# Kernel optimization log

Hardware: AMD Instinct MI355X
Metric: run time of the kernel (lower is better)

The kernel has to match this reference:

```python
import jax, jax.numpy as jnp
import numpy as np

DIM_M = 512
NEG_INF = -1e30


def setup_inputs() -> dict:
    key = jax.random.key(0)
    k1, k2, k3, k4, k5, k6, k7 = jax.random.split(key, 7)
    B, Lc, Lq, d = 16, 1024, 512, DIM_M
    C = jax.random.normal(k1, (B, Lc, d), dtype=jnp.float32)
    Q = jax.random.normal(k2, (B, Lq, d), dtype=jnp.float32)
    cmask = jax.random.randint(k3, (B, Lc), 0, 2).astype(jnp.float32)
    qmask = jax.random.randint(k4, (B, Lq), 0, 2).astype(jnp.float32)
    lim = np.sqrt(1.0 / d)
    w = jax.random.uniform(k5, (3 * d,), minval=-lim, maxval=lim, dtype=jnp.float32)
    # out_linear: Linear(4d -> d), torch default init
    bound = np.sqrt(1.0 / (4 * d))
    out_w = jax.random.uniform(k6, (d, 4 * d), minval=-bound, maxval=bound, dtype=jnp.float32)
    out_b = jax.random.uniform(k7, (d,), minval=-bound, maxval=bound, dtype=jnp.float32)
    return {"C": C, "Q": Q, "cmask": cmask, "qmask": qmask, "w": w, "out_w": out_w, "out_b": out_b}


def _mask_logits(t, m):
    return t * m + (1.0 - m) * NEG_INF


def reference(C, Q, cmask, qmask, w, out_w, out_b):
    d = C.shape[-1]
    w1, w2, w3 = w[:d], w[d:2 * d], w[2 * d:]
    # Decomposed trilinear similarity (same math as cat([Ct,Qt,Ct*Qt]) @ w):
    # S[b,i,j] = C[b,i]@w1 + Q[b,j]@w2 + (C[b,i]*w3) @ Q[b,j]
    S = (C @ w1)[:, :, None] + (Q @ w2)[:, None, :] \
        + jnp.einsum('bid,bjd->bij', C * w3, Q)  # [B, Lc, Lq]
    qm = qmask[:, None, :]  # [B, 1, Lq]
    cm = cmask[:, :, None]  # [B, Lc, 1]
    S1 = jax.nn.softmax(_mask_logits(S, qm), axis=2)  # over Lq
    S2 = jax.nn.softmax(_mask_logits(S, cm), axis=1)  # over Lc
    A = jnp.einsum('bij,bjd->bid', S1, Q)  # [B, Lc, d]
    # bmm(bmm(S1, S2^T), C) == S1 @ (S2^T @ C) by associativity (cheaper)
    S2TC = jnp.einsum('bij,bid->bjd', S2, C)  # [B, Lq, d]
    Bm = jnp.einsum('bij,bjd->bid', S1, S2TC)  # [B, Lc, d]
    out = jnp.concatenate([C, A, C * A, C * Bm], axis=2)  # [B, Lc, 4d]
    # dropout inactive (inference); out_linear
    return out @ out_w.T + out_b
```

## Files before the change

kernel.cpp:

```cpp
#include <hip/hip_runtime.h>
#include <hip/hip_bf16.h>


#define NB 16
#define LC 1024
#define LQ 512
#define DM 512
#define D4 2048
#define NEGINF (-1e30f)
#define LDA64 72
#define LDA32 40

typedef __bf16 v8bf __attribute__((ext_vector_type(8)));
typedef __bf16 v4bf __attribute__((ext_vector_type(4)));
typedef float  v4f  __attribute__((ext_vector_type(4)));

#define MFMA16 __builtin_amdgcn_mfma_f32_16x16x32_bf16

#define TILE_SETUP8 \
  const int t = threadIdx.x, lane = t & 63, wave = t >> 6; \
  const int wm = wave >> 2, wn = wave & 3, quad = lane >> 4, col = lane & 15;

#define ZERO_ACC8 \
  v4f acc[4][2]; \
  _Pragma("unroll") for (int x = 0; x < 4; ++x) \
  _Pragma("unroll") for (int y = 0; y < 2; ++y) \
  _Pragma("unroll") for (int r = 0; r < 4; ++r) acc[x][y][r] = 0.f;

#define FRAG_MMA8S(AL, BL, LDA, KO) do { \
  v8bf af_[4], bf_[2]; \
  _Pragma("unroll") for (int x = 0; x < 4; ++x) \
    af_[x] = *(const v8bf*)&AL[(wm * 64 + x * 16 + col) * LDA + KO + quad * 8]; \
  _Pragma("unroll") for (int y = 0; y < 2; ++y) \
    bf_[y] = *(const v8bf*)&BL[(wn * 32 + y * 16 + col) * LDA + KO + quad * 8]; \
  _Pragma("unroll") for (int x = 0; x < 4; ++x) \
  _Pragma("unroll") for (int y = 0; y < 2; ++y) \
    acc[x][y] = MFMA16(af_[x], bf_[y], acc[x][y], 0, 0, 0); \
} while (0)

#define TILE_SETUP4 \
  const int t = threadIdx.x, lane = t & 63, wave = t >> 6; \
  const int wm = wave >> 1, wn = wave & 1, quad = lane >> 4, col = lane & 15;

#define ZERO_ACC4 \
  v4f acc[4][4]; \
  _Pragma("unroll") for (int x = 0; x < 4; ++x) \
  _Pragma("unroll") for (int y = 0; y < 4; ++y) \
  _Pragma("unroll") for (int r = 0; r < 4; ++r) acc[x][y][r] = 0.f;

#define FRAG_MMA4(AL, BL, LDA, KO) do { \
  v8bf af_[4], bf_[4]; \
  _Pragma("unroll") for (int x = 0; x < 4; ++x) \
    af_[x] = *(const v8bf*)&AL[(wm * 64 + x * 16 + col) * LDA + KO + quad * 8]; \
  _Pragma("unroll") for (int y = 0; y < 4; ++y) \
    bf_[y] = *(const v8bf*)&BL[(wn * 64 + y * 16 + col) * LDA + KO + quad * 8]; \
  _Pragma("unroll") for (int x = 0; x < 4; ++x) \
  _Pragma("unroll") for (int y = 0; y < 4; ++y) \
    acc[x][y] = MFMA16(af_[x], bf_[y], acc[x][y], 0, 0, 0); \
} while (0)

__device__ __forceinline__ void xcd_remap(int& bx, int& by, int& bz) {
  const int gx = gridDim.x, gy = gridDim.y, gz = gridDim.z;
  int flat = bx + gx * (by + gy * bz);
  int per = (gx * gy * gz) >> 3;
  int nw = (flat & 7) * per + (flat >> 3);
  bx = nw % gx;
  int r = nw / gx;
  by = r % gy;
  bz = r / gy;
}

__device__ __forceinline__ v8bf cvt8f(float4 a, float4 b) {
  v8bf h;
  h[0] = (__bf16)a.x; h[1] = (__bf16)a.y; h[2] = (__bf16)a.z; h[3] = (__bf16)a.w;
  h[4] = (__bf16)b.x; h[5] = (__bf16)b.y; h[6] = (__bf16)b.z; h[7] = (__bf16)b.w;
  return h;
}

__global__ void k_transpose(const float* __restrict__ in, __bf16* __restrict__ outT,
                            int R, int Cd) {
  __shared__ __bf16 tile[64][66];
  const int b = blockIdx.z;
  const int r0 = blockIdx.y * 64, c0 = blockIdx.x * 64;
  const float* inb = in + (size_t)b * R * Cd;
  __bf16* outb = outT + (size_t)b * Cd * R;
  const int rr = threadIdx.x >> 4, c4 = (threadIdx.x & 15) * 4;
#pragma unroll
  for (int p = 0; p < 4; ++p) {
    const int r = rr + p * 16;
    float4 f = *(const float4*)(inb + (size_t)(r0 + r) * Cd + c0 + c4);
    tile[r][c4 + 0] = (__bf16)f.x; tile[r][c4 + 1] = (__bf16)f.y;
    tile[r][c4 + 2] = (__bf16)f.z; tile[r][c4 + 3] = (__bf16)f.w;
  }
  __syncthreads();
  const int c = threadIdx.x & 63, rb = (threadIdx.x >> 6) * 4;
#pragma unroll
  for (int p = 0; p < 4; ++p) {
    const int r4 = rb + p * 16;
    v4bf h;
#pragma unroll
    for (int e = 0; e < 4; ++e) h[e] = tile[r4 + e][c];
    *(v4bf*)(outb + (size_t)(c0 + c) * R + r0 + r4) = h;
  }
}

__global__ void k_owcvt(const float* __restrict__ OW, __bf16* __restrict__ OWb) {
  size_t i = ((size_t)blockIdx.x * 256 + threadIdx.x) * 4;
  float4 f = *(const float4*)(OW + i);
  v4bf h; h[0] = (__bf16)f.x; h[1] = (__bf16)f.y; h[2] = (__bf16)f.z; h[3] = (__bf16)f.w;
  *(v4bf*)(OWb + i) = h;
}

__global__ __launch_bounds__(512) void k_mfma_S(
    const float* __restrict__ C, const float* __restrict__ Q, const float* __restrict__ w,
    float* __restrict__ S) {
  __shared__ __bf16 Al[128 * LDA64], Bl[128 * LDA64];
  __shared__ float cwL[128], qwL[128];
  int bx = blockIdx.x, by = blockIdx.y, bz = blockIdx.z;
  xcd_remap(bx, by, bz);
  const int b = bz, i0 = by * 128, j0 = bx * 128;
  TILE_SETUP8
  const int sr = t >> 2, skc = (t & 3) * 16;
  const float* Cb = C + (size_t)b * LC * DM;
  const float* Qb = Q + (size_t)b * LQ * DM;
  const float* w1 = w, *w2 = w + DM, *w3 = w + 2 * DM;
  float4 pc[4], pq[4];
  auto load = [&](int k0) {
    const float* ca = Cb + (size_t)(i0 + sr) * DM + k0 + skc;
    const float* qa = Qb + (size_t)(j0 + sr) * DM + k0 + skc;
#pragma unroll
    for (int u = 0; u < 4; ++u) {
      pc[u] = *(const float4*)(ca + 4 * u);
      pq[u] = *(const float4*)(qa + 4 * u);
    }
  };
  load(0);
  ZERO_ACC8
  float cdot = 0.f, qdot = 0.f;
  for (int k0 = 0; k0 < DM; k0 += 64) {
#pragma unroll
    for (int u = 0; u < 2; ++u) {
      float4 c0 = pc[2 * u], c1 = pc[2 * u + 1];
      float4 q0 = pq[2 * u], q1 = pq[2 * u + 1];
      const float* w3a = w3 + k0 + skc + 8 * u;
      float4 w30 = *(const float4*)w3a, w31 = *(const float4*)(w3a + 4);
      const float* w1a = w1 + k0 + skc + 8 * u;
      float4 w10 = *(const float4*)w1a, w11 = *(const float4*)(w1a + 4);
      const float* w2a = w2 + k0 + skc + 8 * u;
      float4 w20 = *(const float4*)w2a, w21 = *(const float4*)(w2a + 4);
      v8bf ah;
      ah[0] = (__bf16)(c0.x * w30.x); ah[1] = (__bf16)(c0.y * w30.y);
      ah[2] = (__bf16)(c0.z * w30.z); ah[3] = (__bf16)(c0.w * w30.w);
      ah[4] = (__bf16)(c1.x * w31.x); ah[5] = (__bf16)(c1.y * w31.y);
      ah[6] = (__bf16)(c1.z * w31.z); ah[7] = (__bf16)(c1.w * w31.w);
      *(v8bf*)&Al[sr * LDA64 + skc + 8 * u] = ah;
      *(v8bf*)&Bl[sr * LDA64 + skc + 8 * u] = cvt8f(q0, q1);
      cdot += c0.x * w10.x + c0.y * w10.y + c0.z * w10.z + c0.w * w10.w
            + c1.x * w11.x + c1.y * w11.y + c1.z * w11.z + c1.w * w11.w;
      qdot += q0.x * w20.x + q0.y * w20.y + q0.z * w20.z + q0.w * w20.w
            + q1.x * w21.x + q1.y * w21.y + q1.z * w21.z + q1.w * w21.w;
    }
    __syncthreads();
    int kn = k0 + 64; if (kn >= DM) kn = 0;
    load(kn);
    FRAG_MMA8S(Al, Bl, LDA64, 0);
    FRAG_MMA8S(Al, Bl, LDA64, 32);
    __syncthreads();
  }
  cdot += __shfl_xor(cdot, 1); cdot += __shfl_xor(cdot, 2);
  qdot += __shfl_xor(qdot, 1); qdot += __shfl_xor(qdot, 2);
  if ((t & 3) == 0) { cwL[sr] = cdot; qwL[sr] = qdot; }
  __syncthreads();
  float* Sb = S + (size_t)b * LC * LQ;
#pragma unroll
  for (int x = 0; x < 4; ++x) {
    const int ml = wm * 64 + x * 16 + quad * 4;
    float cv[4];
#pragma unroll
    for (int r = 0; r < 4; ++r) cv[r] = cwL[ml + r];
#pragma unroll
    for (int y = 0; y < 2; ++y) {
      const int jl = wn * 32 + y * 16 + col;
      const float qv = qwL[jl];
#pragma unroll
      for (int r = 0; r < 4; ++r)
        Sb[(size_t)(i0 + ml + r) * LQ + j0 + jl] = acc[x][y][r] + cv[r] + qv;
    }
  }
}

__global__ __launch_bounds__(1024) void k_softstat(
    const float* __restrict__ S, const float* __restrict__ qmask,
    const float* __restrict__ cmask, __bf16* __restrict__ S1,
    float2* __restrict__ pstat) {
  __shared__ float2 cst[16][LQ];
  const int b = blockIdx.y, ic = blockIdx.x;
  const int tid = threadIdx.x, wv = tid >> 6, lane = tid & 63;
  const int jb = lane * 8;
  const float* qm  = qmask + b * LQ;
  const float* cm  = cmask + b * LC + ic * 64;
  const float* Sb  = S  + ((size_t)b * LC + ic * 64) * LQ;
  __bf16*      S1b = S1 + ((size_t)b * LC + ic * 64) * LQ;
  float qv[8];
  {
    float4 q0 = *(const float4*)(qm + jb), q1 = *(const float4*)(qm + jb + 4);
    qv[0] = q0.x; qv[1] = q0.y; qv[2] = q0.z; qv[3] = q0.w;
    qv[4] = q1.x; qv[5] = q1.y; qv[6] = q1.z; qv[7] = q1.w;
  }
  float colm[8], cols[8];
#pragma unroll
  for (int e = 0; e < 8; ++e) { colm[e] = -3e38f; cols[e] = 0.f; }
  for (int it = 0; it < 4; ++it) {
    const int r = wv * 4 + it;
    const float cmv = cm[r];
    const float* Srow = Sb + (size_t)r * LQ + jb;
    float4 s0 = *(const float4*)Srow, s1 = *(const float4*)(Srow + 4);
    float sv[8] = {s0.x, s0.y, s0.z, s0.w, s1.x, s1.y, s1.z, s1.w};
    float l1[8];
    float m = -3e38f;
#pragma unroll
    for (int e = 0; e < 8; ++e) {
      l1[e] = qv[e] * sv[e] + (1.f - qv[e]) * NEGINF;
      m = fmaxf(m, l1[e]);
    }
#pragma unroll
    for (int off = 32; off; off >>= 1) m = fmaxf(m, __shfl_xor(m, off, 64));
    float ex[8], s = 0.f;
#pragma unroll
    for (int e = 0; e < 8; ++e) { ex[e] = __expf(l1[e] - m); s += ex[e]; }
#pragma unroll
    for (int off = 32; off; off >>= 1) s += __shfl_xor(s, off, 64);
    const float inv = 1.f / s;
    v8bf h;
#pragma unroll
    for (int e = 0; e < 8; ++e) h[e] = (__bf16)(ex[e] * inv);
    *(v8bf*)(S1b + (size_t)r * LQ + jb) = h;
#pragma unroll
    for (int e = 0; e < 8; ++e) {
      float l2 = cmv * sv[e] + (1.f - cmv) * NEGINF;
      if (l2 > colm[e]) { cols[e] *= __expf(colm[e] - l2); colm[e] = l2; }
      cols[e] += __expf(l2 - colm[e]);
    }
  }
#pragma unroll
  for (int e = 0; e < 8; ++e) cst[wv][jb + e] = make_float2(colm[e], cols[e]);
  __syncthreads();
  if (tid < LQ) {
    float M = -3e38f, Sd = 0.f;
#pragma unroll
    for (int k = 0; k < 16; ++k) {
      float2 p = cst[k][tid];
      float nM = fmaxf(M, p.x);
      Sd = Sd * __expf(M - nM) + p.y * __expf(p.x - nM);
      M = nM;
    }
    pstat[((size_t)(b * 16 + ic) * LQ) + tid] = make_float2(M, Sd);
  }
}

__global__ void k_colwrite(const float* __restrict__ S, const float* __restrict__ cmask,
                           const float2* __restrict__ pstat, __bf16* __restrict__ S2T) {
  __shared__ float Mf[64], If[64];
  __shared__ __bf16 tile[64][66];
  const int b = blockIdx.z, ic = blockIdx.y, j0 = blockIdx.x * 64;
  if (threadIdx.x < 64) {
    float M = -3e38f, Sd = 0.f;
#pragma unroll
    for (int k = 0; k < 16; ++k) {
      float2 p = pstat[((size_t)(b * 16 + k) * LQ) + j0 + threadIdx.x];
      float nM = fmaxf(M, p.x);
      Sd = Sd * __expf(M - nM) + p.y * __expf(p.x - nM);
      M = nM;
    }
    Mf[threadIdx.x] = M; If[threadIdx.x] = 1.f / Sd;
  }
  __syncthreads();
  const float* Sb = S + ((size_t)b * LC + ic * 64) * LQ;
  const float* cm = cmask + b * LC + ic * 64;
  const int rr = threadIdx.x >> 4, c4 = (threadIdx.x & 15) * 4;
#pragma unroll
  for (int p = 0; p < 4; ++p) {
    const int r = rr + p * 16;
    const float mk = cm[r];
    float4 sv = *(const float4*)(Sb + (size_t)r * LQ + j0 + c4);
    float s[4] = {sv.x, sv.y, sv.z, sv.w};
#pragma unroll
    for (int e = 0; e < 4; ++e) {
      float logit = mk * s[e] + (1.f - mk) * NEGINF;
      tile[r][c4 + e] = (__bf16)(__expf(logit - Mf[c4 + e]) * If[c4 + e]);
    }
  }
  __syncthreads();
  __bf16* S2Tb = S2T + ((size_t)b * LQ + j0) * LC + ic * 64;
  const int c = threadIdx.x & 63, rb = (threadIdx.x >> 6) * 4;
#pragma unroll
  for (int p = 0; p < 4; ++p) {
    const int r4 = rb + p * 16;
    v4bf h;
#pragma unroll
    for (int e = 0; e < 4; ++e) h[e] = tile[r4 + e][c];
    *(v4bf*)(S2Tb + (size_t)c * LC + r4) = h;
  }
}

__global__ __launch_bounds__(256) void k_mfma_A(
    const __bf16* __restrict__ S1, const __bf16* __restrict__ QT, __bf16* __restrict__ Aw) {
  __shared__ __bf16 Al[128 * LDA64], Bl[128 * LDA64];
  int bx = blockIdx.x, by = blockIdx.y, bz = blockIdx.z;
  xcd_remap(bx, by, bz);
  const int b = bz, i0 = by * 128, n0 = bx * 128;
  TILE_SETUP4
  const int sr = t >> 1, kh = (t & 1) * 32;
  const __bf16* Ar = S1 + (size_t)b * LC * LQ + (size_t)(i0 + sr) * LQ + kh;
  const __bf16* Br = QT + (size_t)b * DM * LQ + (size_t)(n0 + sr) * LQ + kh;
  v8bf pa[4], pb[4];
  auto load = [&](int k0) {
#pragma unroll
    for (int u = 0; u < 4; ++u) {
      pa[u] = *(const v8bf*)(Ar + k0 + 8 * u);
      pb[u] = *(const v8bf*)(Br + k0 + 8 * u);
    }
  };
  load(0);
  ZERO_ACC4
  for (int k0 = 0; k0 < LQ; k0 += 64) {
#pragma unroll
    for (int u = 0; u < 4; ++u) {
      *(v8bf*)&Al[sr * LDA64 + kh + 8 * u] = pa[u];
      *(v8bf*)&Bl[sr * LDA64 + kh + 8 * u] = pb[u];
    }
    __syncthreads();
    int kn = k0 + 64; if (kn >= LQ) kn = 0;
    load(kn);
    FRAG_MMA4(Al, Bl, LDA64, 0);
    FRAG_MMA4(Al, Bl, LDA64, 32);
    __syncthreads();
  }
  __bf16* Ab = Aw + (size_t)b * LC * DM;
#pragma unroll
  for (int x = 0; x < 4; ++x) {
    const int mB = i0 + wm * 64 + x * 16 + quad * 4;
#pragma unroll
    for (int y = 0; y < 4; ++y) {
      const int n = n0 + wn * 64 + y * 16 + col;
#pragma unroll
      for (int r = 0; r < 4; ++r)
        Ab[(size_t)(mB + r) * DM + n] = (__bf16)acc[x][y][r];
    }
  }
}

__global__ __launch_bounds__(512) void k_mfma_T(
    const __bf16* __restrict__ S2T, const __bf16* __restrict__ CT, __bf16* __restrict__ S2TCT) {
  __shared__ __bf16 Al[128 * LDA64], Bl[128 * LDA64];
  int bx = blockIdx.x, by = blockIdx.y, bz = blockIdx.z;
  xcd_remap(bx, by, bz);
  const int b = bz, j0 = by * 128, n0 = bx * 128;
  TILE_SETUP8
  const int sr = t >> 2, skc = (t & 3) * 16;
  const __bf16* Ar = S2T + (size_t)b * LQ * LC + (size_t)(j0 + sr) * LC + skc;
  const __bf16* Br = CT  + (size_t)b * DM * LC + (size_t)(n0 + sr) * LC + skc;
  v8bf pa0, pa1, pb0, pb1;
  auto load = [&](int k0) {
    pa0 = *(const v8bf*)(Ar + k0); pa1 = *(const v8bf*)(Ar + k0 + 8);
    pb0 = *(const v8bf*)(Br + k0); pb1 = *(const v8bf*)(Br + k0 + 8);
  };
  load(0);
  ZERO_ACC8
  for (int k0 = 0; k0 < LC; k0 += 64) {
    *(v8bf*)&Al[sr * LDA64 + skc] = pa0; *(v8bf*)&Al[sr * LDA64 + skc + 8] = pa1;
    *(v8bf*)&Bl[sr * LDA64 + skc] = pb0; *(v8bf*)&Bl[sr * LDA64 + skc + 8] = pb1;
    __syncthreads();
    int kn = k0 + 64; if (kn >= LC) kn = 0;
    load(kn);
    FRAG_MMA8S(Al, Bl, LDA64, 0);
    FRAG_MMA8S(Al, Bl, LDA64, 32);
    __syncthreads();
  }
#pragma unroll
  for (int x = 0; x < 4; ++x) {
    const int jB = j0 + wm * 64 + x * 16 + quad * 4;
#pragma unroll
    for (int y = 0; y < 2; ++y) {
      const int n = n0 + wn * 32 + y * 16 + col;
      v4bf h;
#pragma unroll
      for (int r = 0; r < 4; ++r) h[r] = (__bf16)acc[x][y][r];
      *(v4bf*)&S2TCT[((size_t)b * DM + n) * LQ + jB] = h;
    }
  }
}

__global__ __launch_bounds__(256) void k_mfma_Bm(
    const __bf16* __restrict__ S1, const __bf16* __restrict__ S2TCT, __bf16* __restrict__ Bmw) {
  __shared__ __bf16 Al[128 * LDA64], Bl[128 * LDA64];
  int bx = blockIdx.x, by = blockIdx.y, bz = blockIdx.z;
  xcd_remap(bx, by, bz);
  const int b = bz, i0 = by * 128, n0 = bx * 128;
  TILE_SETUP4
  const int sr = t >> 1, kh = (t & 1) * 32;
  const __bf16* Ar = S1    + (size_t)b * LC * LQ + (size_t)(i0 + sr) * LQ + kh;
  const __bf16* Br = S2TCT + (size_t)b * DM * LQ + (size_t)(n0 + sr) * LQ + kh;
  v8bf pa[4], pb[4];
  auto load = [&](int k0) {
#pragma unroll
    for (int u = 0; u < 4; ++u) {
      pa[u] = *(const v8bf*)(Ar + k0 + 8 * u);
      pb[u] = *(const v8bf*)(Br + k0 + 8 * u);
    }
  };
  load(0);
  ZERO_ACC4
  for (int k0 = 0; k0 < LQ; k0 += 64) {
#pragma unroll
    for (int u = 0; u < 4; ++u) {
      *(v8bf*)&Al[sr * LDA64 + kh + 8 * u] = pa[u];
      *(v8bf*)&Bl[sr * LDA64 + kh + 8 * u] = pb[u];
    }
    __syncthreads();
    int kn = k0 + 64; if (kn >= LQ) kn = 0;
    load(kn);
    FRAG_MMA4(Al, Bl, LDA64, 0);
    FRAG_MMA4(Al, Bl, LDA64, 32);
    __syncthreads();
  }
  __bf16* Bb = Bmw + (size_t)b * LC * DM;
#pragma unroll
  for (int x = 0; x < 4; ++x) {
    const int mB = i0 + wm * 64 + x * 16 + quad * 4;
#pragma unroll
    for (int y = 0; y < 4; ++y) {
      const int n = n0 + wn * 64 + y * 16 + col;
#pragma unroll
      for (int r = 0; r < 4; ++r)
        Bb[(size_t)(mB + r) * DM + n] = (__bf16)acc[x][y][r];
    }
  }
}

__global__ __launch_bounds__(256) void k_mfma_out(
    const float* __restrict__ C, const __bf16* __restrict__ Aw, const __bf16* __restrict__ Bmw,
    const __bf16* __restrict__ OWb, const float* __restrict__ ob, float* __restrict__ out) {
  __shared__ __bf16 Asg[4][128 * LDA32], Bsg[4][128 * LDA32];
  int bx = blockIdx.x, by = blockIdx.y, bz = blockIdx.z;
  xcd_remap(bx, by, bz);
  const int b = bz, i0 = by * 128, n0 = bx * 128;
  TILE_SETUP4
  const int sr = t >> 1, kh = (t & 1) * 16;
  const float*  Cr = C   + (size_t)b * LC * DM + (size_t)(i0 + sr) * DM + kh;
  const __bf16* Ar = Aw  + (size_t)b * LC * DM + (size_t)(i0 + sr) * DM + kh;
  const __bf16* Br = Bmw + (size_t)b * LC * DM + (size_t)(i0 + sr) * DM + kh;
  const __bf16* Wr = OWb + (size_t)(n0 + sr) * D4 + kh;
  float4 pc[4]; v8bf pA[2], pB[2], pw[4][2];
  auto load = [&](int kl) {
#pragma unroll
    for (int u = 0; u < 4; ++u) pc[u] = *(const float4*)(Cr + kl + 4 * u);
#pragma unroll
    for (int u = 0; u < 2; ++u) {
      pA[u] = *(const v8bf*)(Ar + kl + 8 * u);
      pB[u] = *(const v8bf*)(Br + kl + 8 * u);
    }
#pragma unroll
    for (int s = 0; s < 4; ++s)
#pragma unroll
      for (int u = 0; u < 2; ++u) pw[s][u] = *(const v8bf*)(Wr + s * DM + kl + 8 * u);
  };
  load(0);
  ZERO_ACC4
  for (int kl = 0; kl < DM; kl += 32) {
#pragma unroll
    for (int u = 0; u < 2; ++u) {
      float4 f0 = pc[2 * u], f1 = pc[2 * u + 1];
      float cf[8] = {f0.x, f0.y, f0.z, f0.w, f1.x, f1.y, f1.z, f1.w};
      v8bf hC, hCA, hCB;
#pragma unroll
      for (int e = 0; e < 8; ++e) {
        hC[e]  = (__bf16)cf[e];
        hCA[e] = (__bf16)(cf[e] * (float)pA[u][e]);
        hCB[e] = (__bf16)(cf[e] * (float)pB[u][e]);
      }
      const int off = sr * LDA32 + kh + 8 * u;
      *(v8bf*)&Asg[0][off] = hC;
      *(v8bf*)&Asg[1][off] = pA[u];
      *(v8bf*)&Asg[2][off] = hCA;
      *(v8bf*)&Asg[3][off] = hCB;
#pragma unroll
      for (int s = 0; s < 4; ++s) *(v8bf*)&Bsg[s][off] = pw[s][u];
    }
    __syncthreads();
    int kn = kl + 32; if (kn >= DM) kn = 0;
    load(kn);
#pragma unroll
    for (int s = 0; s < 4; ++s) FRAG_MMA4(Asg[s], Bsg[s], LDA32, 0);
    __syncthreads();
  }
  float* outb = out + (size_t)b * LC * DM;
#pragma unroll
  for (int x = 0; x < 4; ++x) {
    const int mB = i0 + wm * 64 + x * 16 + quad * 4;
#pragma unroll
    for (int y = 0; y < 4; ++y) {
      const int n = n0 + wn * 64 + y * 16 + col;
      const float bv = ob[n];
#pragma unroll
      for (int r = 0; r < 4; ++r)
        outb[(size_t)(mB + r) * DM + n] = acc[x][y][r] + bv;
    }
  }
}

extern "C" void kernel_launch(void* const* d_in, const int* in_sizes, int n_in,
                              void* d_out, int out_size, void* d_ws, size_t ws_size,
                              hipStream_t stream) {
  const float* C     = (const float*)d_in[0];
  const float* Q     = (const float*)d_in[1];
  const float* cmask = (const float*)d_in[2];
  const float* qmask = (const float*)d_in[3];
  const float* w     = (const float*)d_in[4];
  const float* out_w = (const float*)d_in[5];
  const float* out_b = (const float*)d_in[6];
  float* out = (float*)d_out;

  char* base = (char*)d_ws;
  char*   R     = base + 131072;
  float*  S     = (float*)R;
  __bf16* Aw    = (__bf16*)R;
  __bf16* CT    = (__bf16*)(R + (16u << 20));
  __bf16* Bmw   = (__bf16*)(R + (16u << 20));
  __bf16* S1    = (__bf16*)(base + 131072 + (32u << 20));
  __bf16* S2T   = (__bf16*)(base + 131072 + (48u << 20));
  __bf16* OWbf  = S2T;
  char*   Z     = base + 131072 + (64u << 20);
  float2* pstat = (float2*)Z;
  __bf16* QT    = (__bf16*)Z;
  __bf16* S2TCT = (__bf16*)Z;
  (void)in_sizes; (void)n_in; (void)out_size; (void)ws_size;

  k_mfma_S<<<dim3(LQ / 128, LC / 128, NB), 512, 0, stream>>>(C, Q, w, S);
  k_softstat<<<dim3(LC / 64, NB), 1024, 0, stream>>>(S, qmask, cmask, S1, pstat);
  k_colwrite<<<dim3(LQ / 64, LC / 64, NB), 256, 0, stream>>>(S, cmask, pstat, S2T);
  k_transpose<<<dim3(DM / 64, LQ / 64, NB), 256, 0, stream>>>(Q, QT, LQ, DM);
  k_transpose<<<dim3(DM / 64, LC / 64, NB), 256, 0, stream>>>(C, CT, LC, DM);
  k_mfma_A<<<dim3(DM / 128, LC / 128, NB), 256, 0, stream>>>(S1, QT, Aw);
  k_mfma_T<<<dim3(DM / 128, LQ / 128, NB), 512, 0, stream>>>(S2T, CT, S2TCT);
  k_owcvt<<<DM * D4 / 1024, 256, 0, stream>>>(out_w, OWbf);
  k_mfma_Bm<<<dim3(DM / 128, LC / 128, NB), 256, 0, stream>>>(S1, S2TCT, Bmw);
  k_mfma_out<<<dim3(DM / 128, LC / 128, NB), 256, 0, stream>>>(C, Aw, Bmw, OWbf, out_b, out);
}
```

Baseline: 315.5 us.

## Use 8-wave tiles for GEMMs and pre-swizzle out_w into MFMA fragment layout

Switches k_mfma_A, k_mfma_Bm and k_mfma_out from 4-wave 64x64 warp tiles to 8-wave 64x32 tiles with 512-thread blocks, halving per-thread accumulators and staging loads. out_w is now pre-converted into MFMA B-fragment order, so k_mfma_out reads weight fragments directly from global memory/cache instead of staging them through LDS. This cuts LDS footprint and traffic. Transpose writes are widened to 16-byte stores. The trade-off is more weight fragment loads from global memory per wave, and smaller per-wave tiles with lower reuse.

```diff
diff --git a/kernel.cpp b/kernel.cpp
--- a/kernel.cpp
+++ b/kernel.cpp
@@ -38,27 +38,6 @@
     acc[x][y] = MFMA16(af_[x], bf_[y], acc[x][y], 0, 0, 0); \
 } while (0)
 
-#define TILE_SETUP4 \
-  const int t = threadIdx.x, lane = t & 63, wave = t >> 6; \
-  const int wm = wave >> 1, wn = wave & 1, quad = lane >> 4, col = lane & 15;
-
-#define ZERO_ACC4 \
-  v4f acc[4][4]; \
-  _Pragma("unroll") for (int x = 0; x < 4; ++x) \
-  _Pragma("unroll") for (int y = 0; y < 4; ++y) \
-  _Pragma("unroll") for (int r = 0; r < 4; ++r) acc[x][y][r] = 0.f;
-
-#define FRAG_MMA4(AL, BL, LDA, KO) do { \
-  v8bf af_[4], bf_[4]; \
-  _Pragma("unroll") for (int x = 0; x < 4; ++x) \
-    af_[x] = *(const v8bf*)&AL[(wm * 64 + x * 16 + col) * LDA + KO + quad * 8]; \
-  _Pragma("unroll") for (int y = 0; y < 4; ++y) \
-    bf_[y] = *(const v8bf*)&BL[(wn * 64 + y * 16 + col) * LDA + KO + quad * 8]; \
-  _Pragma("unroll") for (int x = 0; x < 4; ++x) \
-  _Pragma("unroll") for (int y = 0; y < 4; ++y) \
-    acc[x][y] = MFMA16(af_[x], bf_[y], acc[x][y], 0, 0, 0); \
-} while (0)
-
 __device__ __forceinline__ void xcd_remap(int& bx, int& by, int& bz) {
   const int gx = gridDim.x, gy = gridDim.y, gz = gridDim.z;
   int flat = bx + gx * (by + gy * bz);
@@ -93,22 +72,23 @@
     tile[r][c4 + 2] = (__bf16)f.z; tile[r][c4 + 3] = (__bf16)f.w;
   }
   __syncthreads();
-  const int c = threadIdx.x & 63, rb = (threadIdx.x >> 6) * 4;
-#pragma unroll
-  for (int p = 0; p < 4; ++p) {
-    const int r4 = rb + p * 16;
-    v4bf h;
-#pragma unroll
-    for (int e = 0; e < 4; ++e) h[e] = tile[r4 + e][c];
-    *(v4bf*)(outb + (size_t)(c0 + c) * R + r0 + r4) = h;
-  }
-}
-
-__global__ void k_owcvt(const float* __restrict__ OW, __bf16* __restrict__ OWb) {
-  size_t i = ((size_t)blockIdx.x * 256 + threadIdx.x) * 4;
-  float4 f = *(const float4*)(OW + i);
-  v4bf h; h[0] = (__bf16)f.x; h[1] = (__bf16)f.y; h[2] = (__bf16)f.z; h[3] = (__bf16)f.w;
-  *(v4bf*)(OWb + i) = h;
+  const int cc = threadIdx.x >> 2, r16 = (threadIdx.x & 3) * 16;
+  v8bf h0, h1;
+#pragma unroll
+  for (int e = 0; e < 8; ++e) { h0[e] = tile[r16 + e][cc]; h1[e] = tile[r16 + 8 + e][cc]; }
+  *(v8bf*)(outb + (size_t)(c0 + cc) * R + r0 + r16) = h0;
+  *(v8bf*)(outb + (size_t)(c0 + cc) * R + r0 + r16 + 8) = h1;
+}
+
+__global__ void k_owfrag(const float* __restrict__ OW, __bf16* __restrict__ Wf) {
+  const int gid = blockIdx.x * 256 + threadIdx.x;
+  const int lane = gid & 63, f = gid >> 6;
+  const int nt = f >> 6, kc = f & 63;
+  const int n = nt * 16 + (lane & 15);
+  const int k = kc * 32 + (lane >> 4) * 8;
+  const float* src = OW + (size_t)n * D4 + k;
+  float4 a = *(const float4*)src, b = *(const float4*)(src + 4);
+  *(v8bf*)(Wf + (size_t)f * 512 + lane * 8) = cvt8f(a, b);
 }
 
 __global__ __launch_bounds__(512) void k_mfma_S(
@@ -292,48 +272,39 @@
   }
   __syncthreads();
   __bf16* S2Tb = S2T + ((size_t)b * LQ + j0) * LC + ic * 64;
-  const int c = threadIdx.x & 63, rb = (threadIdx.x >> 6) * 4;
-#pragma unroll
-  for (int p = 0; p < 4; ++p) {
-    const int r4 = rb + p * 16;
-    v4bf h;
-#pragma unroll
-    for (int e = 0; e < 4; ++e) h[e] = tile[r4 + e][c];
-    *(v4bf*)(S2Tb + (size_t)c * LC + r4) = h;
-  }
-}
-
-__global__ __launch_bounds__(256) void k_mfma_A(
+  const int jj = threadIdx.x >> 2, i16 = (threadIdx.x & 3) * 16;
+  v8bf h0, h1;
+#pragma unroll
+  for (int e = 0; e < 8; ++e) { h0[e] = tile[i16 + e][jj]; h1[e] = tile[i16 + 8 + e][jj]; }
+  *(v8bf*)(S2Tb + (size_t)jj * LC + i16) = h0;
+  *(v8bf*)(S2Tb + (size_t)jj * LC + i16 + 8) = h1;
+}
+
+__global__ __launch_bounds__(512) void k_mfma_A(
     const __bf16* __restrict__ S1, const __bf16* __restrict__ QT, __bf16* __restrict__ Aw) {
   __shared__ __bf16 Al[128 * LDA64], Bl[128 * LDA64];
   int bx = blockIdx.x, by = blockIdx.y, bz = blockIdx.z;
   xcd_remap(bx, by, bz);
   const int b = bz, i0 = by * 128, n0 = bx * 128;
-  TILE_SETUP4
-  const int sr = t >> 1, kh = (t & 1) * 32;
-  const __bf16* Ar = S1 + (size_t)b * LC * LQ + (size_t)(i0 + sr) * LQ + kh;
-  const __bf16* Br = QT + (size_t)b * DM * LQ + (size_t)(n0 + sr) * LQ + kh;
-  v8bf pa[4], pb[4];
+  TILE_SETUP8
+  const int sr = t >> 2, skc = (t & 3) * 16;
+  const __bf16* Ar = S1 + (size_t)b * LC * LQ + (size_t)(i0 + sr) * LQ + skc;
+  const __bf16* Br = QT + (size_t)b * DM * LQ + (size_t)(n0 + sr) * LQ + skc;
+  v8bf pa0, pa1, pb0, pb1;
   auto load = [&](int k0) {
-#pragma unroll
-    for (int u = 0; u < 4; ++u) {
-      pa[u] = *(const v8bf*)(Ar + k0 + 8 * u);
-      pb[u] = *(const v8bf*)(Br + k0 + 8 * u);
-    }
+    pa0 = *(const v8bf*)(Ar + k0); pa1 = *(const v8bf*)(Ar + k0 + 8);
+    pb0 = *(const v8bf*)(Br + k0); pb1 = *(const v8bf*)(Br + k0 + 8);
   };
   load(0);
-  ZERO_ACC4
+  ZERO_ACC8
   for (int k0 = 0; k0 < LQ; k0 += 64) {
-#pragma unroll
-    for (int u = 0; u < 4; ++u) {
-      *(v8bf*)&Al[sr * LDA64 + kh + 8 * u] = pa[u];
-      *(v8bf*)&Bl[sr * LDA64 + kh + 8 * u] = pb[u];
-    }
+    *(v8bf*)&Al[sr * LDA64 + skc] = pa0; *(v8bf*)&Al[sr * LDA64 + skc + 8] = pa1;
+    *(v8bf*)&Bl[sr * LDA64 + skc] = pb0; *(v8bf*)&Bl[sr * LDA64 + skc + 8] = pb1;
     __syncthreads();
     int kn = k0 + 64; if (kn >= LQ) kn = 0;
     load(kn);
-    FRAG_MMA4(Al, Bl, LDA64, 0);
-    FRAG_MMA4(Al, Bl, LDA64, 32);
+    FRAG_MMA8S(Al, Bl, LDA64, 0);
+    FRAG_MMA8S(Al, Bl, LDA64, 32);
     __syncthreads();
   }
   __bf16* Ab = Aw + (size_t)b * LC * DM;
@@ -341,8 +312,8 @@
   for (int x = 0; x < 4; ++x) {
     const int mB = i0 + wm * 64 + x * 16 + quad * 4;
 #pragma unroll
-    for (int y = 0; y < 4; ++y) {
-      const int n = n0 + wn * 64 + y * 16 + col;
+    for (int y = 0; y < 2; ++y) {
+      const int n = n0 + wn * 32 + y * 16 + col;
 #pragma unroll
       for (int r = 0; r < 4; ++r)
         Ab[(size_t)(mB + r) * DM + n] = (__bf16)acc[x][y][r];
@@ -391,37 +362,31 @@
   }
 }
 
-__global__ __launch_bounds__(256) void k_mfma_Bm(
+__global__ __launch_bounds__(512) void k_mfma_Bm(
     const __bf16* __restrict__ S1, const __bf16* __restrict__ S2TCT, __bf16* __restrict__ Bmw) {
   __shared__ __bf16 Al[128 * LDA64], Bl[128 * LDA64];
   int bx = blockIdx.x, by = blockIdx.y, bz = blockIdx.z;
   xcd_remap(bx, by, bz);
   const int b = bz, i0 = by * 128, n0 = bx * 128;
-  TILE_SETUP4
-  const int sr = t >> 1, kh = (t & 1) * 32;
-  const __bf16* Ar = S1    + (size_t)b * LC * LQ + (size_t)(i0 + sr) * LQ + kh;
-  const __bf16* Br = S2TCT + (size_t)b * DM * LQ + (size_t)(n0 + sr) * LQ + kh;
-  v8bf pa[4], pb[4];
+  TILE_SETUP8
+  const int sr = t >> 2, skc = (t & 3) * 16;
+  const __bf16* Ar = S1    + (size_t)b * LC * LQ + (size_t)(i0 + sr) * LQ + skc;
+  const __bf16* Br = S2TCT + (size_t)b * DM * LQ + (size_t)(n0 + sr) * LQ + skc;
+  v8bf pa0, pa1, pb0, pb1;
   auto load = [&](int k0) {
-#pragma unroll
-    for (int u = 0; u < 4; ++u) {
-      pa[u] = *(const v8bf*)(Ar + k0 + 8 * u);
-      pb[u] = *(const v8bf*)(Br + k0 + 8 * u);
-    }
+    pa0 = *(const v8bf*)(Ar + k0); pa1 = *(const v8bf*)(Ar + k0 + 8);
+    pb0 = *(const v8bf*)(Br + k0); pb1 = *(const v8bf*)(Br + k0 + 8);
   };
   load(0);
-  ZERO_ACC4
+  ZERO_ACC8
   for (int k0 = 0; k0 < LQ; k0 += 64) {
-#pragma unroll
-    for (int u = 0; u < 4; ++u) {
-      *(v8bf*)&Al[sr * LDA64 + kh + 8 * u] = pa[u];
-      *(v8bf*)&Bl[sr * LDA64 + kh + 8 * u] = pb[u];
-    }
+    *(v8bf*)&Al[sr * LDA64 + skc] = pa0; *(v8bf*)&Al[sr * LDA64 + skc + 8] = pa1;
+    *(v8bf*)&Bl[sr * LDA64 + skc] = pb0; *(v8bf*)&Bl[sr * LDA64 + skc + 8] = pb1;
     __syncthreads();
     int kn = k0 + 64; if (kn >= LQ) kn = 0;
     load(kn);
-    FRAG_MMA4(Al, Bl, LDA64, 0);
-    FRAG_MMA4(Al, Bl, LDA64, 32);
+    FRAG_MMA8S(Al, Bl, LDA64, 0);
+    FRAG_MMA8S(Al, Bl, LDA64, 32);
     __syncthreads();
   }
   __bf16* Bb = Bmw + (size_t)b * LC * DM;
@@ -429,8 +394,8 @@
   for (int x = 0; x < 4; ++x) {
     const int mB = i0 + wm * 64 + x * 16 + quad * 4;
 #pragma unroll
-    for (int y = 0; y < 4; ++y) {
-      const int n = n0 + wn * 64 + y * 16 + col;
+    for (int y = 0; y < 2; ++y) {
+      const int n = n0 + wn * 32 + y * 16 + col;
 #pragma unroll
       for (int r = 0; r < 4; ++r)
         Bb[(size_t)(mB + r) * DM + n] = (__bf16)acc[x][y][r];
@@ -438,60 +403,64 @@
   }
 }
 
-__global__ __launch_bounds__(256) void k_mfma_out(
+__global__ __launch_bounds__(512) void k_mfma_out(
     const float* __restrict__ C, const __bf16* __restrict__ Aw, const __bf16* __restrict__ Bmw,
-    const __bf16* __restrict__ OWb, const float* __restrict__ ob, float* __restrict__ out) {
-  __shared__ __bf16 Asg[4][128 * LDA32], Bsg[4][128 * LDA32];
+    const __bf16* __restrict__ Wf, const float* __restrict__ ob, float* __restrict__ out) {
+  __shared__ __bf16 Asg[4][128 * LDA32];
   int bx = blockIdx.x, by = blockIdx.y, bz = blockIdx.z;
   xcd_remap(bx, by, bz);
   const int b = bz, i0 = by * 128, n0 = bx * 128;
-  TILE_SETUP4
-  const int sr = t >> 1, kh = (t & 1) * 16;
-  const float*  Cr = C   + (size_t)b * LC * DM + (size_t)(i0 + sr) * DM + kh;
-  const __bf16* Ar = Aw  + (size_t)b * LC * DM + (size_t)(i0 + sr) * DM + kh;
-  const __bf16* Br = Bmw + (size_t)b * LC * DM + (size_t)(i0 + sr) * DM + kh;
-  const __bf16* Wr = OWb + (size_t)(n0 + sr) * D4 + kh;
-  float4 pc[4]; v8bf pA[2], pB[2], pw[4][2];
+  TILE_SETUP8
+  const int sr = t >> 2, skc = (t & 3) * 8;
+  const float*  Cr = C   + (size_t)b * LC * DM + (size_t)(i0 + sr) * DM + skc;
+  const __bf16* Ar = Aw  + (size_t)b * LC * DM + (size_t)(i0 + sr) * DM + skc;
+  const __bf16* Br = Bmw + (size_t)b * LC * DM + (size_t)(i0 + sr) * DM + skc;
+  const int ntb = n0 >> 4;
+  float4 pc0, pc1; v8bf pA, pB;
   auto load = [&](int kl) {
-#pragma unroll
-    for (int u = 0; u < 4; ++u) pc[u] = *(const float4*)(Cr + kl + 4 * u);
-#pragma unroll
-    for (int u = 0; u < 2; ++u) {
-      pA[u] = *(const v8bf*)(Ar + kl + 8 * u);
-      pB[u] = *(const v8bf*)(Br + kl + 8 * u);
-    }
-#pragma unroll
-    for (int s = 0; s < 4; ++s)
-#pragma unroll
-      for (int u = 0; u < 2; ++u) pw[s][u] = *(const v8bf*)(Wr + s * DM + kl + 8 * u);
+    pc0 = *(const float4*)(Cr + kl); pc1 = *(const float4*)(Cr + kl + 4);
+    pA = *(const v8bf*)(Ar + kl);
+    pB = *(const v8bf*)(Br + kl);
   };
   load(0);
-  ZERO_ACC4
+  ZERO_ACC8
   for (int kl = 0; kl < DM; kl += 32) {
-#pragma unroll
-    for (int u = 0; u < 2; ++u) {
-      float4 f0 = pc[2 * u], f1 = pc[2 * u + 1];
-      float cf[8] = {f0.x, f0.y, f0.z, f0.w, f1.x, f1.y, f1.z, f1.w};
-      v8bf hC, hCA, hCB;
-#pragma unroll
-      for (int e = 0; e < 8; ++e) {
-        hC[e]  = (__bf16)cf[e];
-        hCA[e] = (__bf16)(cf[e] * (float)pA[u][e]);
-        hCB[e] = (__bf16)(cf[e] * (float)pB[u][e]);
-      }
-      const int off = sr * LDA32 + kh + 8 * u;
-      *(v8bf*)&Asg[0][off] = hC;
-      *(v8bf*)&Asg[1][off] = pA[u];
-      *(v8bf*)&Asg[2][off] = hCA;
-      *(v8bf*)&Asg[3][off] = hCB;
-#pragma unroll
-      for (int s = 0; s < 4; ++s) *(v8bf*)&Bsg[s][off] = pw[s][u];
-    }
+    float cf[8] = {pc0.x, pc0.y, pc0.z, pc0.w, pc1.x, pc1.y, pc1.z, pc1.w};
+    v8bf hC, hCA, hCB;
+#pragma unroll
+    for (int e = 0; e < 8; ++e) {
+      hC[e]  = (__bf16)cf[e];
+      hCA[e] = (__bf16)(cf[e] * (float)pA[e]);
+      hCB[e] = (__bf16)(cf[e] * (float)pB[e]);
+    }
+    const int off = sr * LDA32 + skc;
+    *(v8bf*)&Asg[0][off] = hC;
+    *(v8bf*)&Asg[1][off] = pA;
+    *(v8bf*)&Asg[2][off] = hCA;
+    *(v8bf*)&Asg[3][off] = hCB;
     __syncthreads();
     int kn = kl + 32; if (kn >= DM) kn = 0;
     load(kn);
-#pragma unroll
-    for (int s = 0; s < 4; ++s) FRAG_MMA4(Asg[s], Bsg[s], LDA32, 0);
+    const int kcb = kl >> 5;
+    v8bf bfr[4][2];
+#pragma unroll
+    for (int s = 0; s < 4; ++s)
+#pragma unroll
+      for (int y = 0; y < 2; ++y)
+        bfr[s][y] = *(const v8bf*)(Wf +
+          (size_t)((ntb + wn * 2 + y) * 64 + s * 16 + kcb) * 512 + lane * 8);
+#pragma unroll
+    for (int s = 0; s < 4; ++s) {
+      v8bf af_[4];
+#pragma unroll
+      for (int x = 0; x < 4; ++x)
+        af_[x] = *(const v8bf*)&Asg[s][(wm * 64 + x * 16 + col) * LDA32 + quad * 8];
+#pragma unroll
+      for (int x = 0; x < 4; ++x) {
+        acc[x][0] = MFMA16(af_[x], bfr[s][0], acc[x][0], 0, 0, 0);
+        acc[x][1] = MFMA16(af_[x], bfr[s][1], acc[x][1], 0, 0, 0);
+      }
+    }
     __syncthreads();
   }
   float* outb = out + (size_t)b * LC * DM;
@@ -499,8 +468,8 @@
   for (int x = 0; x < 4; ++x) {
     const int mB = i0 + wm * 64 + x * 16 + quad * 4;
 #pragma unroll
-    for (int y = 0; y < 4; ++y) {
-      const int n = n0 + wn * 64 + y * 16 + col;
+    for (int y = 0; y < 2; ++y) {
+      const int n = n0 + wn * 32 + y * 16 + col;
       const float bv = ob[n];
 #pragma unroll
       for (int r = 0; r < 4; ++r)
@@ -522,18 +491,18 @@
   float* out = (float*)d_out;
 
   char* base = (char*)d_ws;
-  char*   R     = base + 131072;
-  float*  S     = (float*)R;
-  __bf16* Aw    = (__bf16*)R;
-  __bf16* CT    = (__bf16*)(R + (16u << 20));
-  __bf16* Bmw   = (__bf16*)(R + (16u << 20));
-  __bf16* S1    = (__bf16*)(base + 131072 + (32u << 20));
-  __bf16* S2T   = (__bf16*)(base + 131072 + (48u << 20));
-  __bf16* OWbf  = S2T;
-  char*   Z     = base + 131072 + (64u << 20);
-  float2* pstat = (float2*)Z;
-  __bf16* QT    = (__bf16*)Z;
-  __bf16* S2TCT = (__bf16*)Z;
+  char*   R      = base + 131072;
+  float*  S      = (float*)R;
+  __bf16* Aw     = (__bf16*)R;
+  __bf16* CT     = (__bf16*)(R + (16u << 20));
+  __bf16* Bmw    = (__bf16*)(R + (16u << 20));
+  __bf16* S1     = (__bf16*)(base + 131072 + (32u << 20));
+  __bf16* S2T    = (__bf16*)(base + 131072 + (48u << 20));
+  __bf16* OWfrag = S2T;
+  char*   Z      = base + 131072 + (64u << 20);
+  float2* pstat  = (float2*)Z;
+  __bf16* QT     = (__bf16*)Z;
+  __bf16* S2TCT  = (__bf16*)Z;
   (void)in_sizes; (void)n_in; (void)out_size; (void)ws_size;
 
   k_mfma_S<<<dim3(LQ / 128, LC / 128, NB), 512, 0, stream>>>(C, Q, w, S);
@@ -541,9 +510,9 @@
   k_colwrite<<<dim3(LQ / 64, LC / 64, NB), 256, 0, stream>>>(S, cmask, pstat, S2T);
   k_transpose<<<dim3(DM / 64, LQ / 64, NB), 256, 0, stream>>>(Q, QT, LQ, DM);
   k_transpose<<<dim3(DM / 64, LC / 64, NB), 256, 0, stream>>>(C, CT, LC, DM);
-  k_mfma_A<<<dim3(DM / 128, LC / 128, NB), 256, 0, stream>>>(S1, QT, Aw);
+  k_mfma_A<<<dim3(DM / 128, LC / 128, NB), 512, 0, stream>>>(S1, QT, Aw);
   k_mfma_T<<<dim3(DM / 128, LQ / 128, NB), 512, 0, stream>>>(S2T, CT, S2TCT);
-  k_owcvt<<<DM * D4 / 1024, 256, 0, stream>>>(out_w, OWbf);
-  k_mfma_Bm<<<dim3(DM / 128, LC / 128, NB), 256, 0, stream>>>(S1, S2TCT, Bmw);
-  k_mfma_out<<<dim3(DM / 128, LC / 128, NB), 256, 0, stream>>>(C, Aw, Bmw, OWbf, out_b, out);
-}
+  k_owfrag<<<512, 256, 0, stream>>>(out_w, OWfrag);
+  k_mfma_Bm<<<dim3(DM / 128, LC / 128, NB), 512, 0, stream>>>(S1, S2TCT, Bmw);
+  k_mfma_out<<<dim3(DM / 128, LC / 128, NB), 512, 0, stream>>>(C, Aw, Bmw, OWfrag, out_b, out);
+}
```

Result: faster. 284.3 us (-9.9%).
